# Performance work log

Hardware: AMD Instinct MI355X
Metric: run time of the kernel (lower is better)

## Reference

```python
import jax, jax.numpy as jnp
import numpy as np
import math

# Model dims
B, S, D, H, G, L = 1, 1024, 1024, 16, 4, 4
HD = D // H            # 64 head dim
DFF = 4 * D            # 4096
V = 32000              # vocab
HPG = H // G           # heads per KV group


def cosine_norm(x):
    n = jnp.maximum(jnp.linalg.norm(x, axis=-1, keepdims=True), 1e-6)
    return x / n


def rope(x):
    # x: (B, heads, S, HD), rotate-half RoPE along seq dim 2
    hd = x.shape[-1]
    s = x.shape[2]
    inv = 1.0 / (10000.0 ** (jnp.arange(0, hd, 2, dtype=jnp.float32) / hd))
    ang = jnp.arange(s, dtype=jnp.float32)[:, None] * inv[None, :]  # (S, hd/2)
    cos = jnp.concatenate([jnp.cos(ang), jnp.cos(ang)], -1)
    sin = jnp.concatenate([jnp.sin(ang), jnp.sin(ang)], -1)
    x1, x2 = jnp.split(x, 2, -1)
    return x * cos + jnp.concatenate([-x2, x1], -1) * sin


def setup_inputs() -> dict:
    key = jax.random.key(0)
    ks = jax.random.split(key, 12)
    w = lambda k, shape: jax.random.normal(k, shape, jnp.float32) * 0.02
    return {
        'x': jax.random.randint(ks[0], (B, S), 0, V),
        'emb': w(ks[1], (V, D)),
        'qw': w(ks[2], (L, D, D)), 'qb': jnp.zeros((L, D)),
        'kw': w(ks[3], (L, G * HD, D)), 'kb': jnp.zeros((L, G * HD)),
        'vw': w(ks[4], (L, G * HD, D)), 'vb': jnp.zeros((L, G * HD)),
        'sqk': jnp.full((L, H, HD), 1.0 / math.sqrt(HD)),
        'ow': w(ks[5], (L, D, D)), 'ob': jnp.zeros((L, D)),
        'w_in': w(ks[6], (L, DFF, D)), 'b_in': jnp.zeros((L, DFF)),
        'w_gate': w(ks[7], (L, DFF, D)), 'b_gate': jnp.zeros((L, DFF)),
        'w_out': w(ks[8], (L, D, DFF)), 'b_out': jnp.zeros((L, D)),
        's_u': jnp.ones((L, DFF)), 's_v': jnp.ones((L, DFF)),
        'eig_a': jnp.full((L, D), 1.0 / math.sqrt(D)),
        'eig_m': jnp.full((L, D), 1.0 / math.sqrt(D)),
        'out_w': w(ks[9], (V, D)), 'out_b': jnp.zeros((V,)),
        's_z': jnp.full((V,), 1.0 / math.sqrt(D)),
    }


def reference(x, emb, qw, qb, kw, kb, vw, vb, sqk, ow, ob, w_in, b_in,
              w_gate, b_gate, w_out, b_out, s_u, s_v, eig_a, eig_m,
              out_w, out_b, s_z):
    h = emb[x]  # (B, S, D)
    causal = jnp.tril(jnp.ones((S, S), dtype=bool))
    rtd = math.sqrt(HD)
    rtD = math.sqrt(D)
    for i in range(L):
        # --- GQA attention with RoPE + cosine-normed QK ---
        q = (jnp.einsum('bsd,ed->bse', h, qw[i]) + qb[i]).reshape(B, S, H, HD).transpose(0, 2, 1, 3)
        k = (jnp.einsum('bsd,ed->bse', h, kw[i]) + kb[i]).reshape(B, S, G, HD).transpose(0, 2, 1, 3)
        v = (jnp.einsum('bsd,ed->bse', h, vw[i]) + vb[i]).reshape(B, S, G, HD).transpose(0, 2, 1, 3)
        q = rope(q)
        k = rope(k)
        k = jnp.repeat(k, HPG, axis=1)  # expand groups -> heads
        v = jnp.repeat(v, HPG, axis=1)
        eff = (sqk[i] * rtd)[None, :, None, :]  # s_qk * (s_qk_init / s_qk_scale)
        q = cosine_norm(q) * eff
        k = cosine_norm(k) * eff
        a = jnp.einsum('bhqd,bhkd->bhqk', q, k) * rtd
        a = jnp.where(causal[None, None], a, -1e9)
        a = jax.nn.softmax(a, axis=-1)
        attn = jnp.einsum('bhqk,bhkd->bhqd', a, v).transpose(0, 2, 1, 3).reshape(B, S, D)
        attn = jnp.einsum('bsd,ed->bse', attn, ow[i]) + ob[i]
        x_a = cosine_norm(attn)
        h = cosine_norm(h + (eig_a[i] * rtD) * (x_a - h))
        # --- SwiGLU FFN ---
        u = (jnp.einsum('bsd,fd->bsf', h, w_in[i]) + b_in[i]) * s_u[i]
        g = (jnp.einsum('bsd,fd->bsf', h, w_gate[i]) + b_gate[i]) * s_v[i] * rtD
        ff = jnp.einsum('bsf,df->bsd', u * jax.nn.silu(g), w_out[i]) + b_out[i]
        x_m = cosine_norm(ff)
        h = cosine_norm(h + (eig_m[i] * rtD) * (x_m - h))
    logits = (jnp.einsum('bsd,vd->bsv', h, out_w) + out_b) * (s_z * rtD)
    return jax.nn.softmax(logits, axis=-1)
```

## Files before the change

### kernel.cpp

```cpp
#include <hip/hip_runtime.h>
#include <cstddef>
#include <cstdint>

#define S_ 1024
#define D_ 1024
#define H_ 16
#define G_ 4
#define HD_ 64
#define DFF_ 4096
#define V_ 32000
#define L_ 4

typedef __bf16 v8bf __attribute__((ext_vector_type(8)));
typedef float f32x4 __attribute__((ext_vector_type(4)));

__device__ __forceinline__ unsigned short f2bf(float x) {
  unsigned u = __float_as_uint(x);
  return (unsigned short)((u + 0x7fffu + ((u >> 16) & 1u)) >> 16);
}

__global__ __launch_bounds__(256) void embed_k(const int* __restrict__ x,
                                               const float* __restrict__ emb,
                                               float* __restrict__ Hv,
                                               unsigned short* __restrict__ Hb) {
  int s = blockIdx.x;
  int r = x[s];
  float4 v = ((const float4*)(emb + (size_t)r * D_))[threadIdx.x];
  ((float4*)(Hv + (size_t)s * D_))[threadIdx.x] = v;
  ((ushort4*)(Hb + (size_t)s * D_))[threadIdx.x] =
      make_ushort4(f2bf(v.x), f2bf(v.y), f2bf(v.z), f2bf(v.w));
}

__global__ __launch_bounds__(256) void f2b_k(const float* __restrict__ in,
                                             unsigned short* __restrict__ out,
                                             int n8) {
  int stride = gridDim.x * 256;
  for (int i = blockIdx.x * 256 + threadIdx.x; i < n8; i += stride) {
    const float4* p = (const float4*)in + 2 * (size_t)i;
    float4 a = p[0], b = p[1];
    ((ushort4*)out)[2 * (size_t)i + 0] = make_ushort4(f2bf(a.x), f2bf(a.y), f2bf(a.z), f2bf(a.w));
    ((ushort4*)out)[2 * (size_t)i + 1] = make_ushort4(f2bf(b.x), f2bf(b.y), f2bf(b.z), f2bf(b.w));
  }
}

__global__ __launch_bounds__(256) void f2b3_k(const float* __restrict__ a,
                                              const float* __restrict__ b,
                                              const float* __restrict__ c,
                                              int na8, int nb8,
                                              unsigned short* __restrict__ out,
                                              int total8) {
  int stride = gridDim.x * 256;
  for (int i = blockIdx.x * 256 + threadIdx.x; i < total8; i += stride) {
    const float* src;
    int j;
    if (i < na8) { src = a; j = i; }
    else if (i < na8 + nb8) { src = b; j = i - na8; }
    else { src = c; j = i - na8 - nb8; }
    float4 x = ((const float4*)src)[2 * (size_t)j];
    float4 y = ((const float4*)src)[2 * (size_t)j + 1];
    ((ushort4*)out)[2 * (size_t)i + 0] = make_ushort4(f2bf(x.x), f2bf(x.y), f2bf(x.z), f2bf(x.w));
    ((ushort4*)out)[2 * (size_t)i + 1] = make_ushort4(f2bf(y.x), f2bf(y.y), f2bf(y.z), f2bf(y.w));
  }
}

__global__ __launch_bounds__(256) void prep_layer(const float* __restrict__ qb,
                                                  const float* __restrict__ kb,
                                                  const float* __restrict__ vb,
                                                  const float* __restrict__ bin,
                                                  const float* __restrict__ bgate,
                                                  const float* __restrict__ su,
                                                  const float* __restrict__ sv,
                                                  float rtD,
                                                  float* __restrict__ qkvb,
                                                  float* __restrict__ ffnb,
                                                  float* __restrict__ ffns) {
  int i = blockIdx.x * 256 + threadIdx.x;
  if (i < 1536)
    qkvb[i] = (i < 1024) ? qb[i] : ((i < 1280) ? kb[i - 1024] : vb[i - 1280]);
  if (i < 8192) {
    ffnb[i] = (i < 4096) ? bin[i] : bgate[i - 4096];
    ffns[i] = (i < 4096) ? su[i] : sv[i - 4096] * rtD;
  }
}

__global__ __launch_bounds__(256) void gemm_bf16(const unsigned short* __restrict__ A,
                                                 const unsigned short* __restrict__ B,
                                                 const float* __restrict__ bias,
                                                 const float* __restrict__ colscale,
                                                 float smul,
                                                 float* __restrict__ C,
                                                 int M, int N, int K) {
  (void)M;
  __shared__ unsigned short As[128 * 64];
  __shared__ unsigned short Bs[128 * 64];
  const int tid = threadIdx.x;
  const int w = tid >> 6;
  const int l = tid & 63;
  const int wm = w >> 1, wn = w & 1;
  const size_t row0 = (size_t)blockIdx.y * 128;
  const size_t col0 = (size_t)blockIdx.x * 128;
  const int fr = l & 15;
  const int kq0 = l >> 4;

  f32x4 acc[4][4];
#pragma unroll
  for (int i = 0; i < 4; ++i)
#pragma unroll
    for (int j = 0; j < 4; ++j) acc[i][j] = (f32x4){0.f, 0.f, 0.f, 0.f};

  for (int k0 = 0; k0 < K; k0 += 64) {
#pragma unroll
    for (int p = 0; p < 4; ++p) {
      const int id = p * 256 + tid;
      const int row = id >> 3;
      const int kbs = (id & 7) ^ (row & 7);
      __builtin_amdgcn_global_load_lds(
          (const __attribute__((address_space(1))) void*)(A + (row0 + row) * K + k0 + kbs * 8),
          (__attribute__((address_space(3))) void*)(As + (size_t)(p * 256 + w * 64) * 8), 16, 0, 0);
      __builtin_amdgcn_global_load_lds(
          (const __attribute__((address_space(1))) void*)(B + (col0 + row) * K + k0 + kbs * 8),
          (__attribute__((address_space(3))) void*)(Bs + (size_t)(p * 256 + w * 64) * 8), 16, 0, 0);
    }
    __syncthreads();
#pragma unroll
    for (int ks = 0; ks < 2; ++ks) {
      v8bf af[4], bfv[4];
      const int kq = ks * 4 + kq0;
#pragma unroll
      for (int i = 0; i < 4; ++i) {
        const int ar = wm * 64 + i * 16 + fr;
        af[i] = *(const v8bf*)(As + ar * 64 + ((kq ^ (ar & 7)) << 3));
        const int br = wn * 64 + i * 16 + fr;
        bfv[i] = *(const v8bf*)(Bs + br * 64 + ((kq ^ (br & 7)) << 3));
      }
#pragma unroll
      for (int i = 0; i < 4; ++i)
#pragma unroll
        for (int j = 0; j < 4; ++j)
          acc[i][j] = __builtin_amdgcn_mfma_f32_16x16x32_bf16(af[i], bfv[j], acc[i][j], 0, 0, 0);
    }
    __syncthreads();
  }

  const int rb = (l >> 4) * 4;
#pragma unroll
  for (int j = 0; j < 4; ++j) {
    const size_t col = col0 + wn * 64 + j * 16 + fr;
    const float bb = bias[col];
    const float cs = (colscale ? colscale[col] : 1.f) * smul;
#pragma unroll
    for (int i = 0; i < 4; ++i) {
      const size_t rowb = row0 + wm * 64 + i * 16 + rb;
#pragma unroll
      for (int r = 0; r < 4; ++r)
        C[(rowb + r) * N + col] = (acc[i][j][r] + bb) * cs;
    }
  }
}

__global__ __launch_bounds__(256) void rope_norm(float* __restrict__ X,
                                                 const float* __restrict__ sqk,
                                                 int NH, int rstride, float rtd) {
  const int idx = blockIdx.x * 4 + (threadIdx.x >> 6);
  const int lane = threadIdx.x & 63;
  const int s = idx / NH, hh = idx - s * NH;
  float* px = X + (size_t)s * rstride + hh * 64;
  float x = px[lane];
  float other = px[lane ^ 32];
  int j = lane & 31;
  float inv = expf(-(float)j * 0.28782313662425572f);
  float ang = (float)s * inv;
  float c = cosf(ang), sn = sinf(ang);
  float rot = (lane < 32) ? -other : other;
  float val = fmaf(x, c, rot * sn);
  float ssq = val * val;
#pragma unroll
  for (int off = 32; off; off >>= 1) ssq += __shfl_xor(ssq, off);
  float scale = 1.0f / fmaxf(sqrtf(ssq), 1e-6f);
  if (sqk) {
    float eff = sqk[hh * 64 + lane] * rtd;
    scale *= eff * eff * rtd;
  }
  px[lane] = val * scale;
}

__global__ __launch_bounds__(256) void attn_fa(const float* __restrict__ QKV,
                                               unsigned short* __restrict__ Ob) {
  const int head = blockIdx.x;
  const int g = head >> 2;
  const int qbase = ((int)gridDim.y - 1 - blockIdx.y) * 16;
  const int tid = threadIdx.x;
  const int w = tid >> 6, lane = tid & 63;
  __shared__ float Ks[64][64];
  __shared__ float Vs[64][64];
  __shared__ float Qs[16][64];
  __shared__ float Ps[16][64];
  {
    int r = tid >> 4, c = (tid & 15) * 4;
    *(float4*)&Qs[r][c] =
        *(const float4*)(QKV + (size_t)(qbase + r) * 1536 + head * 64 + c);
  }
  float m[4], l[4], acc[4];
#pragma unroll
  for (int qi = 0; qi < 4; ++qi) { m[qi] = -1e30f; l[qi] = 0.f; acc[qi] = 0.f; }
  const int q0 = qbase + w * 4;
  const int kbmax = qbase >> 6;
  const int sr = tid >> 2;
  const int sc = tid & 3;

  for (int kb = 0; kb <= kbmax; ++kb) {
    __syncthreads();
    const float* kr = QKV + (size_t)(kb * 64 + sr) * 1536 + 1024 + g * 64;
    const float* vr = kr + 256;
#pragma unroll
    for (int j = 0; j < 4; ++j) {
      int ch = sc * 4 + j;
      *(float4*)&Ks[sr][((ch ^ (sr & 15)) * 4)] = *(const float4*)(kr + ch * 4);
      *(float4*)&Vs[sr][ch * 4] = *(const float4*)(vr + ch * 4);
    }
    __syncthreads();
    float4 kreg[16];
#pragma unroll
    for (int c = 0; c < 16; ++c)
      kreg[c] = *(const float4*)&Ks[lane][((c ^ (lane & 15)) * 4)];
    float s[4] = {0.f, 0.f, 0.f, 0.f};
#pragma unroll
    for (int c = 0; c < 16; ++c) {
#pragma unroll
      for (int qi = 0; qi < 4; ++qi) {
        float4 qv = *(const float4*)&Qs[w * 4 + qi][c * 4];
        s[qi] = fmaf(qv.x, kreg[c].x, s[qi]);
        s[qi] = fmaf(qv.y, kreg[c].y, s[qi]);
        s[qi] = fmaf(qv.z, kreg[c].z, s[qi]);
        s[qi] = fmaf(qv.w, kreg[c].w, s[qi]);
      }
    }
    const int key = kb * 64 + lane;
#pragma unroll
    for (int qi = 0; qi < 4; ++qi) {
      float sv = (key > q0 + qi) ? -1e30f : s[qi];
      float bm = sv;
#pragma unroll
      for (int off = 32; off; off >>= 1) bm = fmaxf(bm, __shfl_xor(bm, off));
      float mnew = fmaxf(m[qi], bm);
      float alpha = __expf(m[qi] - mnew);
      float p = __expf(sv - mnew);
      float ps = p;
#pragma unroll
      for (int off = 32; off; off >>= 1) ps += __shfl_xor(ps, off);
      l[qi] = l[qi] * alpha + ps;
      m[qi] = mnew;
      Ps[w * 4 + qi][lane] = p;
      acc[qi] *= alpha;
    }
#pragma unroll 4
    for (int k4 = 0; k4 < 16; ++k4) {
      float4 pv0 = *(const float4*)&Ps[w * 4 + 0][k4 * 4];
      float4 pv1 = *(const float4*)&Ps[w * 4 + 1][k4 * 4];
      float4 pv2 = *(const float4*)&Ps[w * 4 + 2][k4 * 4];
      float4 pv3 = *(const float4*)&Ps[w * 4 + 3][k4 * 4];
#pragma unroll
      for (int j = 0; j < 4; ++j) {
        float v = Vs[k4 * 4 + j][lane];
        acc[0] = fmaf(((const float*)&pv0)[j], v, acc[0]);
        acc[1] = fmaf(((const float*)&pv1)[j], v, acc[1]);
        acc[2] = fmaf(((const float*)&pv2)[j], v, acc[2]);
        acc[3] = fmaf(((const float*)&pv3)[j], v, acc[3]);
      }
    }
  }
#pragma unroll
  for (int qi = 0; qi < 4; ++qi)
    Ob[(size_t)(q0 + qi) * 1024 + head * 64 + lane] = f2bf(acc[qi] / l[qi]);
}

__global__ __launch_bounds__(256) void resid_norm(float* __restrict__ H,
                                                  unsigned short* __restrict__ Hb,
                                                  const float* __restrict__ Xin,
                                                  const float* __restrict__ eig,
                                                  float rtD) {
  const int row = blockIdx.x, t = threadIdx.x;
  __shared__ float sm1[4], sm2[4];
  float4 xv = *(const float4*)(Xin + (size_t)row * D_ + t * 4);
  float4 hv = *(const float4*)(H + (size_t)row * D_ + t * 4);
  float ss = xv.x * xv.x + xv.y * xv.y + xv.z * xv.z + xv.w * xv.w;
#pragma unroll
  for (int off = 32; off; off >>= 1) ss += __shfl_xor(ss, off);
  if ((t & 63) == 0) sm1[t >> 6] = ss;
  __syncthreads();
  ss = sm1[0] + sm1[1] + sm1[2] + sm1[3];
  float inv1 = 1.0f / fmaxf(sqrtf(ss), 1e-6f);
  float4 ev = *(const float4*)(eig + t * 4);
  float y[4];
  y[0] = hv.x + ev.x * rtD * (xv.x * inv1 - hv.x);
  y[1] = hv.y + ev.y * rtD * (xv.y * inv1 - hv.y);
  y[2] = hv.z + ev.z * rtD * (xv.z * inv1 - hv.z);
  y[3] = hv.w + ev.w * rtD * (xv.w * inv1 - hv.w);
  float s2 = y[0] * y[0] + y[1] * y[1] + y[2] * y[2] + y[3] * y[3];
#pragma unroll
  for (int off = 32; off; off >>= 1) s2 += __shfl_xor(s2, off);
  if ((t & 63) == 0) sm2[t >> 6] = s2;
  __syncthreads();
  s2 = sm2[0] + sm2[1] + sm2[2] + sm2[3];
  float inv2 = 1.0f / fmaxf(sqrtf(s2), 1e-6f);
  float4 o = make_float4(y[0] * inv2, y[1] * inv2, y[2] * inv2, y[3] * inv2);
  *(float4*)(H + (size_t)row * D_ + t * 4) = o;
  ((ushort4*)(Hb + (size_t)row * D_))[t] =
      make_ushort4(f2bf(o.x), f2bf(o.y), f2bf(o.z), f2bf(o.w));
}

__global__ __launch_bounds__(256) void swiglu(const float* __restrict__ UG,
                                              unsigned short* __restrict__ Ub) {
  int i = blockIdx.x * 256 + threadIdx.x;
  int s = i >> 10;
  int f4 = i & 1023;
  float4 u = *(const float4*)(UG + (size_t)s * 8192 + f4 * 4);
  float4 g = *(const float4*)(UG + (size_t)s * 8192 + 4096 + f4 * 4);
  u.x *= g.x / (1.f + __expf(-g.x));
  u.y *= g.y / (1.f + __expf(-g.y));
  u.z *= g.z / (1.f + __expf(-g.z));
  u.w *= g.w / (1.f + __expf(-g.w));
  ((ushort4*)Ub)[(size_t)s * 1024 + f4] = make_ushort4(f2bf(u.x), f2bf(u.y), f2bf(u.z), f2bf(u.w));
}

__global__ __launch_bounds__(256) void softmax_rows(float* __restrict__ X, int N) {
  const int row = blockIdx.x, t = threadIdx.x;
  float* xr = X + (size_t)row * N;
  __shared__ float sm1[4], sm2[4];
  float m = -1e30f;
  for (int c = t; c < N; c += 256) m = fmaxf(m, xr[c]);
#pragma unroll
  for (int off = 32; off; off >>= 1) m = fmaxf(m, __shfl_xor(m, off));
  if ((t & 63) == 0) sm1[t >> 6] = m;
  __syncthreads();
  m = fmaxf(fmaxf(sm1[0], sm1[1]), fmaxf(sm1[2], sm1[3]));
  float l = 0.f;
  for (int c = t; c < N; c += 256) l += __expf(xr[c] - m);
#pragma unroll
  for (int off = 32; off; off >>= 1) l += __shfl_xor(l, off);
  if ((t & 63) == 0) sm2[t >> 6] = l;
  __syncthreads();
  l = sm2[0] + sm2[1] + sm2[2] + sm2[3];
  float inv = 1.0f / l;
  for (int c = t; c < N; c += 256) xr[c] = __expf(xr[c] - m) * inv;
}

extern "C" void kernel_launch(void* const* d_in, const int* in_sizes, int n_in,
                              void* d_out, int out_size, void* d_ws, size_t ws_size,
                              hipStream_t stream) {
  (void)in_sizes; (void)n_in; (void)out_size; (void)ws_size;
  const int*   x      = (const int*)d_in[0];
  const float* emb    = (const float*)d_in[1];
  const float* qw     = (const float*)d_in[2];
  const float* qbias  = (const float*)d_in[3];
  const float* kw     = (const float*)d_in[4];
  const float* kbias  = (const float*)d_in[5];
  const float* vw     = (const float*)d_in[6];
  const float* vbias  = (const float*)d_in[7];
  const float* sqk    = (const float*)d_in[8];
  const float* ow     = (const float*)d_in[9];
  const float* obias  = (const float*)d_in[10];
  const float* w_in   = (const float*)d_in[11];
  const float* b_in   = (const float*)d_in[12];
  const float* w_gate = (const float*)d_in[13];
  const float* b_gate = (const float*)d_in[14];
  const float* w_out  = (const float*)d_in[15];
  const float* b_out  = (const float*)d_in[16];
  const float* s_u    = (const float*)d_in[17];
  const float* s_v    = (const float*)d_in[18];
  const float* eig_a  = (const float*)d_in[19];
  const float* eig_m  = (const float*)d_in[20];
  const float* out_w  = (const float*)d_in[21];
  const float* out_b  = (const float*)d_in[22];
  const float* s_z    = (const float*)d_in[23];
  float* out = (float*)d_out;

  const float rtd = 8.0f;
  const float rtD = 32.0f;

  float* hbuf  = (float*)d_ws;
  float* qkvb  = hbuf + (size_t)S_ * D_;
  float* tbuf  = qkvb + (size_t)S_ * 1536;
  float* ugbuf = tbuf + (size_t)S_ * D_;
  float* pqkv  = ugbuf + (size_t)S_ * 8192;
  float* pffb  = pqkv + 1536;
  float* pffs  = pffb + 8192;
  unsigned short* hb  = (unsigned short*)(pffs + 8192);
  unsigned short* ab  = hb + (size_t)S_ * D_;
  unsigned short* ub  = ab + (size_t)S_ * D_;
  unsigned short* wbf = ub + (size_t)S_ * DFF_;

  auto conv = [&](const float* src, size_t n, unsigned short* dst) {
    int n8 = (int)(n / 8);
    int grid = (n8 + 255) / 256;
    if (grid > 2048) grid = 2048;
    f2b_k<<<grid, 256, 0, stream>>>(src, dst, n8);
  };

  embed_k<<<S_, 256, 0, stream>>>(x, emb, hbuf, hb);

  const int qk8 = (D_ * D_) / 8;
  const int kv8 = (G_ * HD_ * D_) / 8;
  const int ff8 = (DFF_ * D_) / 8;

  for (int i = 0; i < L_; ++i) {
    prep_layer<<<32, 256, 0, stream>>>(
        qbias + (size_t)i * D_, kbias + (size_t)i * G_ * HD_, vbias + (size_t)i * G_ * HD_,
        b_in + (size_t)i * DFF_, b_gate + (size_t)i * DFF_,
        s_u + (size_t)i * DFF_, s_v + (size_t)i * DFF_, rtD, pqkv, pffb, pffs);
    f2b3_k<<<768, 256, 0, stream>>>(qw + (size_t)i * D_ * D_,
                                    kw + (size_t)i * G_ * HD_ * D_,
                                    vw + (size_t)i * G_ * HD_ * D_,
                                    qk8, kv8, wbf, qk8 + 2 * kv8);
    gemm_bf16<<<dim3(1536 / 128, S_ / 128), 256, 0, stream>>>(
        hb, wbf, pqkv, nullptr, 1.0f, qkvb, S_, 1536, D_);
    rope_norm<<<S_ * H_ / 4, 256, 0, stream>>>(qkvb, sqk + (size_t)i * H_ * HD_, H_, 1536, rtd);
    rope_norm<<<S_ * G_ / 4, 256, 0, stream>>>(qkvb + 1024, nullptr, G_, 1536, rtd);
    attn_fa<<<dim3(H_, S_ / 16), 256, 0, stream>>>(qkvb, ab);
    conv(ow + (size_t)i * D_ * D_, (size_t)D_ * D_, wbf);
    gemm_bf16<<<dim3(D_ / 128, S_ / 128), 256, 0, stream>>>(
        ab, wbf, obias + (size_t)i * D_, nullptr, 1.0f, tbuf, S_, D_, D_);
    resid_norm<<<S_, 256, 0, stream>>>(hbuf, hb, tbuf, eig_a + (size_t)i * D_, rtD);
    f2b3_k<<<2048, 256, 0, stream>>>(w_in + (size_t)i * DFF_ * D_,
                                     w_gate + (size_t)i * DFF_ * D_,
                                     w_gate + (size_t)i * DFF_ * D_,
                                     ff8, ff8, wbf, 2 * ff8);
    gemm_bf16<<<dim3(8192 / 128, S_ / 128), 256, 0, stream>>>(
        hb, wbf, pffb, pffs, 1.0f, ugbuf, S_, 8192, D_);
    swiglu<<<(S_ * DFF_) / 1024, 256, 0, stream>>>(ugbuf, ub);
    conv(w_out + (size_t)i * D_ * DFF_, (size_t)D_ * DFF_, wbf);
    gemm_bf16<<<dim3(D_ / 128, S_ / 128), 256, 0, stream>>>(
        ub, wbf, b_out + (size_t)i * D_, nullptr, 1.0f, tbuf, S_, D_, DFF_);
    resid_norm<<<S_, 256, 0, stream>>>(hbuf, hb, tbuf, eig_m + (size_t)i * D_, rtD);
  }

  conv(out_w, (size_t)V_ * D_, wbf);
  gemm_bf16<<<dim3(V_ / 128, S_ / 128), 256, 0, stream>>>(
      hb, wbf, out_b, s_z, rtD, out, S_, V_, D_);
  softmax_rows<<<S_, 256, 0, stream>>>(out, V_);
}
```

Baseline: 1.748 ms.

## Fuse partial softmax stats into LM-head GEMM epilogue and remap workgroups per XCD

The vocab GEMM epilogue now computes per-row partial max and sum-of-exp for each 64-column slice and writes them to scratch reused from the qkv buffer. A new combine kernel merges these partials online and normalizes the logits in one pass, replacing the three-pass row softmax over 32000 columns. All GEMMs also remap workgroup IDs so consecutive tiles land on the same XCD and share L2. This adds shuffle and exp work to the LM-head epilogue, and the remap changes the tile order for every GEMM.

```diff
diff --git a/kernel.cpp b/kernel.cpp
--- a/kernel.cpp
+++ b/kernel.cpp
@@ -89,6 +89,9 @@
                                                  const float* __restrict__ colscale,
                                                  float smul,
                                                  float* __restrict__ C,
+                                                 float* __restrict__ pmax,
+                                                 float* __restrict__ psum,
+                                                 int P,
                                                  int M, int N, int K) {
   (void)M;
   __shared__ unsigned short As[128 * 64];
@@ -97,8 +100,15 @@
   const int w = tid >> 6;
   const int l = tid & 63;
   const int wm = w >> 1, wn = w & 1;
-  const size_t row0 = (size_t)blockIdx.y * 128;
-  const size_t col0 = (size_t)blockIdx.x * 128;
+  const int nwg = (int)(gridDim.x * gridDim.y);
+  const int orig = (int)(blockIdx.y * gridDim.x + blockIdx.x);
+  const int qq = nwg >> 3, rr = nwg & 7;
+  const int xcd = orig & 7, wi = orig >> 3;
+  const int wgid = (xcd < rr ? xcd * (qq + 1) : rr * (qq + 1) + (xcd - rr) * qq) + wi;
+  const int bx = wgid / (int)gridDim.y;
+  const int by = wgid - bx * (int)gridDim.y;
+  const size_t row0 = (size_t)by * 128;
+  const size_t col0 = (size_t)bx * 128;
   const int fr = l & 15;
   const int kq0 = l >> 4;
 
@@ -143,18 +153,81 @@
   }
 
   const int rb = (l >> 4) * 4;
+  float bb[4], cs[4];
 #pragma unroll
   for (int j = 0; j < 4; ++j) {
     const size_t col = col0 + wn * 64 + j * 16 + fr;
-    const float bb = bias[col];
-    const float cs = (colscale ? colscale[col] : 1.f) * smul;
-#pragma unroll
-    for (int i = 0; i < 4; ++i) {
-      const size_t rowb = row0 + wm * 64 + i * 16 + rb;
-#pragma unroll
-      for (int r = 0; r < 4; ++r)
-        C[(rowb + r) * N + col] = (acc[i][j][r] + bb) * cs;
-    }
+    bb[j] = bias[col];
+    cs[j] = (colscale ? colscale[col] : 1.f) * smul;
+  }
+#pragma unroll
+  for (int i = 0; i < 4; ++i) {
+    const size_t rowb = row0 + wm * 64 + i * 16 + rb;
+#pragma unroll
+    for (int r = 0; r < 4; ++r) {
+      float v[4];
+#pragma unroll
+      for (int j = 0; j < 4; ++j) {
+        v[j] = (acc[i][j][r] + bb[j]) * cs[j];
+        C[(rowb + r) * N + col0 + wn * 64 + j * 16 + fr] = v[j];
+      }
+      if (pmax) {
+        float rm = fmaxf(fmaxf(v[0], v[1]), fmaxf(v[2], v[3]));
+#pragma unroll
+        for (int off = 1; off < 16; off <<= 1) rm = fmaxf(rm, __shfl_xor(rm, off));
+        float rs = __expf(v[0] - rm) + __expf(v[1] - rm) + __expf(v[2] - rm) + __expf(v[3] - rm);
+#pragma unroll
+        for (int off = 1; off < 16; off <<= 1) rs += __shfl_xor(rs, off);
+        if (fr == 0) {
+          const size_t pidx = (rowb + r) * P + bx * 2 + wn;
+          pmax[pidx] = rm;
+          psum[pidx] = rs;
+        }
+      }
+    }
+  }
+}
+
+__global__ __launch_bounds__(256) void softmax_combine(float* __restrict__ X,
+                                                       const float* __restrict__ pmax,
+                                                       const float* __restrict__ psum,
+                                                       int N, int P) {
+  const int row = blockIdx.x, t = threadIdx.x;
+  const int w = t >> 6, lane = t & 63;
+  __shared__ float smm[4], sll[4];
+  float m = -1e30f, l = 0.f;
+  for (int p = t; p < P; p += 256) {
+    float bm = pmax[(size_t)row * P + p];
+    float bl = psum[(size_t)row * P + p];
+    float M2 = fmaxf(m, bm);
+    l = l * __expf(m - M2) + bl * __expf(bm - M2);
+    m = M2;
+  }
+#pragma unroll
+  for (int off = 32; off; off >>= 1) {
+    float om = __shfl_xor(m, off), ol = __shfl_xor(l, off);
+    float M2 = fmaxf(m, om);
+    l = l * __expf(m - M2) + ol * __expf(om - M2);
+    m = M2;
+  }
+  if (lane == 0) { smm[w] = m; sll[w] = l; }
+  __syncthreads();
+  m = smm[0]; l = sll[0];
+#pragma unroll
+  for (int k = 1; k < 4; ++k) {
+    float M2 = fmaxf(m, smm[k]);
+    l = l * __expf(m - M2) + sll[k] * __expf(smm[k] - M2);
+    m = M2;
+  }
+  const float inv = 1.0f / l;
+  float4* xr = (float4*)(X + (size_t)row * N);
+  for (int c = t; c < N / 4; c += 256) {
+    float4 v = xr[c];
+    v.x = __expf(v.x - m) * inv;
+    v.y = __expf(v.y - m) * inv;
+    v.z = __expf(v.z - m) * inv;
+    v.w = __expf(v.w - m) * inv;
+    xr[c] = v;
   }
 }
 
@@ -321,28 +394,6 @@
   u.z *= g.z / (1.f + __expf(-g.z));
   u.w *= g.w / (1.f + __expf(-g.w));
   ((ushort4*)Ub)[(size_t)s * 1024 + f4] = make_ushort4(f2bf(u.x), f2bf(u.y), f2bf(u.z), f2bf(u.w));
-}
-
-__global__ __launch_bounds__(256) void softmax_rows(float* __restrict__ X, int N) {
-  const int row = blockIdx.x, t = threadIdx.x;
-  float* xr = X + (size_t)row * N;
-  __shared__ float sm1[4], sm2[4];
-  float m = -1e30f;
-  for (int c = t; c < N; c += 256) m = fmaxf(m, xr[c]);
-#pragma unroll
-  for (int off = 32; off; off >>= 1) m = fmaxf(m, __shfl_xor(m, off));
-  if ((t & 63) == 0) sm1[t >> 6] = m;
-  __syncthreads();
-  m = fmaxf(fmaxf(sm1[0], sm1[1]), fmaxf(sm1[2], sm1[3]));
-  float l = 0.f;
-  for (int c = t; c < N; c += 256) l += __expf(xr[c] - m);
-#pragma unroll
-  for (int off = 32; off; off >>= 1) l += __shfl_xor(l, off);
-  if ((t & 63) == 0) sm2[t >> 6] = l;
-  __syncthreads();
-  l = sm2[0] + sm2[1] + sm2[2] + sm2[3];
-  float inv = 1.0f / l;
-  for (int c = t; c < N; c += 256) xr[c] = __expf(xr[c] - m) * inv;
 }
 
 extern "C" void kernel_launch(void* const* d_in, const int* in_sizes, int n_in,
@@ -385,6 +436,8 @@
   float* pqkv  = ugbuf + (size_t)S_ * 8192;
   float* pffb  = pqkv + 1536;
   float* pffs  = pffb + 8192;
+  float* pmax  = qkvb;
+  float* psum  = qkvb + (size_t)S_ * 500;
   unsigned short* hb  = (unsigned short*)(pffs + 8192);
   unsigned short* ab  = hb + (size_t)S_ * D_;
   unsigned short* ub  = ab + (size_t)S_ * D_;
@@ -413,29 +466,29 @@
                                     vw + (size_t)i * G_ * HD_ * D_,
                                     qk8, kv8, wbf, qk8 + 2 * kv8);
     gemm_bf16<<<dim3(1536 / 128, S_ / 128), 256, 0, stream>>>(
-        hb, wbf, pqkv, nullptr, 1.0f, qkvb, S_, 1536, D_);
+        hb, wbf, pqkv, nullptr, 1.0f, qkvb, nullptr, nullptr, 0, S_, 1536, D_);
     rope_norm<<<S_ * H_ / 4, 256, 0, stream>>>(qkvb, sqk + (size_t)i * H_ * HD_, H_, 1536, rtd);
     rope_norm<<<S_ * G_ / 4, 256, 0, stream>>>(qkvb + 1024, nullptr, G_, 1536, rtd);
     attn_fa<<<dim3(H_, S_ / 16), 256, 0, stream>>>(qkvb, ab);
     conv(ow + (size_t)i * D_ * D_, (size_t)D_ * D_, wbf);
     gemm_bf16<<<dim3(D_ / 128, S_ / 128), 256, 0, stream>>>(
-        ab, wbf, obias + (size_t)i * D_, nullptr, 1.0f, tbuf, S_, D_, D_);
+        ab, wbf, obias + (size_t)i * D_, nullptr, 1.0f, tbuf, nullptr, nullptr, 0, S_, D_, D_);
     resid_norm<<<S_, 256, 0, stream>>>(hbuf, hb, tbuf, eig_a + (size_t)i * D_, rtD);
     f2b3_k<<<2048, 256, 0, stream>>>(w_in + (size_t)i * DFF_ * D_,
                                      w_gate + (size_t)i * DFF_ * D_,
                                      w_gate + (size_t)i * DFF_ * D_,
                                      ff8, ff8, wbf, 2 * ff8);
     gemm_bf16<<<dim3(8192 / 128, S_ / 128), 256, 0, stream>>>(
-        hb, wbf, pffb, pffs, 1.0f, ugbuf, S_, 8192, D_);
+        hb, wbf, pffb, pffs, 1.0f, ugbuf, nullptr, nullptr, 0, S_, 8192, D_);
     swiglu<<<(S_ * DFF_) / 1024, 256, 0, stream>>>(ugbuf, ub);
     conv(w_out + (size_t)i * D_ * DFF_, (size_t)D_ * DFF_, wbf);
     gemm_bf16<<<dim3(D_ / 128, S_ / 128), 256, 0, stream>>>(
-        ub, wbf, b_out + (size_t)i * D_, nullptr, 1.0f, tbuf, S_, D_, DFF_);
+        ub, wbf, b_out + (size_t)i * D_, nullptr, 1.0f, tbuf, nullptr, nullptr, 0, S_, D_, DFF_);
     resid_norm<<<S_, 256, 0, stream>>>(hbuf, hb, tbuf, eig_m + (size_t)i * D_, rtD);
   }
 
   conv(out_w, (size_t)V_ * D_, wbf);
   gemm_bf16<<<dim3(V_ / 128, S_ / 128), 256, 0, stream>>>(
-      hb, wbf, out_b, s_z, rtD, out, S_, V_, D_);
-  softmax_rows<<<S_, 256, 0, stream>>>(out, V_);
-}
+      hb, wbf, out_b, s_z, rtD, out, pmax, psum, 500, S_, V_, D_);
+  softmax_combine<<<S_, 256, 0, stream>>>(out, pmax, psum, V_, 500);
+}
```

After: 1.670 ms. -4.5%, faster.
